# Optimization experiments

Hardware: AMD Instinct MI355X
Metric: run time of the kernel (lower is better)

Reference implementation:

```python
import jax, jax.numpy as jnp
import numpy as np
from jax import lax

B_SZ, C_IN, C_OUT, H_IM, W_IM = 2, 128, 128, 64, 64
N_STATE = 16
DT_RANK = 4  # ceil(128/32)


def _ln_cf(x, w, b, eps=1e-6):
    # channels_first LayerNorm over channel dim
    u = x.mean(1, keepdims=True)
    s = ((x - u) ** 2).mean(1, keepdims=True)
    return w[None, :, None, None] * (x - u) / jnp.sqrt(s + eps) + b[None, :, None, None]


def _bn_train(x, g, b, eps=1e-5):
    # BatchNorm2d in training mode (batch statistics, biased variance)
    m = x.mean((0, 2, 3), keepdims=True)
    v = ((x - m) ** 2).mean((0, 2, 3), keepdims=True)
    return g[None, :, None, None] * (x - m) / jnp.sqrt(v + eps) + b[None, :, None, None]


def _dwconv(x, w, b):
    y = lax.conv_general_dilated(x, w, (1, 1), 'SAME', feature_group_count=x.shape[1],
                                 dimension_numbers=('NCHW', 'OIHW', 'NCHW'))
    return y + b[None, :, None, None]


def _conv1x1(x, w, b):
    return jnp.einsum('oi,bihw->bohw', w, x) + b[None, :, None, None]


def _selective_scan(u, dt, A, Bm, Cm, D, delta_bias):
    # u, dt: [B,Ch,L]; A: [Ch,N]; Bm, Cm: [B,N,L]; D: [Ch]
    dt = jax.nn.softplus(dt + delta_bias[None, :, None])
    xs = (dt.transpose(2, 0, 1), u.transpose(2, 0, 1), Bm.transpose(2, 0, 1), Cm.transpose(2, 0, 1))
    h0 = jnp.zeros(u.shape[:2] + (A.shape[1],), u.dtype)

    def step(h, inp):
        dt_t, u_t, b_t, c_t = inp
        dA = jnp.exp(dt_t[..., None] * A)                        # [B,Ch,N]
        h = h * dA + (dt_t * u_t)[..., None] * b_t[:, None, :]   # [B,Ch,N]
        return h, jnp.einsum('bcn,bn->bc', h, c_t)

    _, ys = lax.scan(step, h0, xs)
    return ys.transpose(1, 2, 0) + u * D[None, :, None]


def _ssm_apply(u, Wx, bx, Wdt, bdt, Alog, D, r):
    # u: [B,Ch,L]. Replicates torch row-major .reshape of [(B L),D] -> [B,D,L].
    Bb, Ch, L = u.shape
    N = Alog.shape[1]
    x_flat = u.transpose(0, 2, 1).reshape(Bb * L, Ch)   # 'b c l -> (b l) c'
    x_dbl = x_flat @ Wx.T + bx
    dt = (x_dbl[:, :r] @ Wdt.T + bdt).reshape(Bb, Wdt.shape[0], L)
    Bm = x_dbl[:, r:r + N].reshape(Bb, N, L)
    Cm = x_dbl[:, r + N:].reshape(Bb, N, L)
    return _selective_scan(u, dt, -jnp.exp(Alog), Bm, Cm, D, bdt)


def _forward(x, ln_in_w, ln_in_b, inproj_w, inproj_b, ln_mamba_w, ln_mamba_b, convm_w, convm_b,
             convr_w, convr_b, ln_cat_w, ln_cat_b, xproj_f_w, xproj_f_b, dtproj_f_w, dtproj_f_b,
             Alog_f, D_f, xproj_b_w, xproj_b_b, dtproj_b_w, dtproj_b_b, Alog_b, D_b,
             xproj_u_w, xproj_u_b, dtproj_u_w, dtproj_u_b, Alog_u, D_u, gate1_w, gate1_b,
             bn_g, bn_b, gate2_w, gate2_b, outproj_w, outproj_b, outln_w, outln_b):
    Bb, C, H, W = x.shape
    L = H * W
    half = C // 2
    x = _ln_cf(x, ln_in_w, ln_in_b)
    xp = _conv1x1(x, inproj_w, inproj_b)
    x_mamba, x_res = xp[:, :C], xp[:, C:]
    x_mamba = _ln_cf(x_mamba, ln_mamba_w, ln_mamba_b)
    x_mamba = jax.nn.silu(_dwconv(x_mamba, convm_w, convm_b))
    x_res = jax.nn.silu(_dwconv(x_res, convr_w, convr_b))
    # forward scan on first half of channels
    xf = x_mamba[:, :half].reshape(Bb, half, L)
    yf = _ssm_apply(xf, xproj_f_w, xproj_f_b, dtproj_f_w, dtproj_f_b, Alog_f, D_f, DT_RANK).reshape(Bb, half, H, W)
    # backward scan on second half (flip H,W, scan, flip back)
    xb = x_mamba[:, half:][:, :, ::-1, ::-1]
    yb = _ssm_apply(xb.reshape(Bb, half, L), xproj_b_w, xproj_b_b, dtproj_b_w, dtproj_b_b,
                    Alog_b, D_b, DT_RANK).reshape(Bb, half, H, W)[:, :, ::-1, ::-1]
    concat = _ln_cf(jnp.concatenate([yf, yb], axis=1), ln_cat_w, ln_cat_b)
    # uncertainty-ordered scan on full x_mamba
    sig = jax.nn.sigmoid(x_mamba.mean(1, keepdims=True))
    unc = (-(sig * jnp.log(sig + 1e-6))).reshape(Bb, L)
    idx = jnp.argsort(-unc, axis=1)       # descending uncertainty
    inv = jnp.argsort(idx, axis=1)        # inverse permutation
    xs = jnp.take_along_axis(x_mamba.reshape(Bb, C, L), idx[:, None, :], axis=2)
    yu = _ssm_apply(xs, xproj_u_w, xproj_u_b, dtproj_u_w, dtproj_u_b, Alog_u, D_u, 2 * DT_RANK)
    yu = jnp.take_along_axis(yu, inv[:, None, :], axis=2).reshape(Bb, C, H, W)
    # gated fusion
    g = jax.nn.relu(_bn_train(_conv1x1(jnp.concatenate([concat, yu], 1), gate1_w, gate1_b), bn_g, bn_b))
    g = jax.nn.sigmoid(_conv1x1(g, gate2_w, gate2_b))
    fused = g * yu + (1.0 - g) * concat
    out = _conv1x1(jnp.concatenate([fused, x_res], 1), outproj_w, outproj_b)
    return _ln_cf(out, outln_w, outln_b)


def setup_inputs() -> dict:
    key = jax.random.key(0)
    ks = jax.random.split(key, 16)
    C, half, R, N = C_IN, C_IN // 2, DT_RANK, N_STATE
    rn = lambda k, shp, s=0.02: jax.random.normal(k, shp, jnp.float32) * s

    def inv_dt(k, n):
        dt = jnp.exp(jax.random.uniform(k, (n,)) * (np.log(0.1) - np.log(0.001)) + np.log(0.001))
        dt = jnp.maximum(dt, 1e-4)
        return dt + jnp.log(-jnp.expm1(-dt))

    std = R ** -0.5
    Alog_h = jnp.log(jnp.broadcast_to(jnp.arange(1, N + 1, dtype=jnp.float32), (half, N)))
    Alog_fl = jnp.log(jnp.broadcast_to(jnp.arange(1, N + 1, dtype=jnp.float32), (C, N)))
    return {
        'x': jax.random.normal(ks[0], (B_SZ, C, H_IM, W_IM), jnp.float32),
        'ln_in_w': jnp.ones(C), 'ln_in_b': jnp.zeros(C),
        'inproj_w': rn(ks[1], (2 * C, C)), 'inproj_b': jnp.zeros(2 * C),
        'ln_mamba_w': jnp.ones(C), 'ln_mamba_b': jnp.zeros(C),
        'convm_w': rn(ks[2], (C, 1, 3, 3), 0.1), 'convm_b': jnp.zeros(C),
        'convr_w': rn(ks[3], (C, 1, 3, 3), 0.1), 'convr_b': jnp.zeros(C),
        'ln_cat_w': jnp.ones(C), 'ln_cat_b': jnp.zeros(C),
        'xproj_f_w': rn(ks[4], (R + 2 * N, half)), 'xproj_f_b': jnp.zeros(R + 2 * N),
        'dtproj_f_w': jax.random.uniform(ks[5], (half, R), minval=-std, maxval=std),
        'dtproj_f_b': inv_dt(ks[6], half),
        'Alog_f': Alog_h, 'D_f': jnp.ones(half),
        'xproj_b_w': rn(ks[7], (R + 2 * N, half)), 'xproj_b_b': jnp.zeros(R + 2 * N),
        'dtproj_b_w': jax.random.uniform(ks[8], (half, R), minval=-std, maxval=std),
        'dtproj_b_b': inv_dt(ks[9], half),
        'Alog_b': Alog_h, 'D_b': jnp.ones(half),
        'xproj_u_w': rn(ks[10], (2 * R + 2 * N, C)), 'xproj_u_b': jnp.zeros(2 * R + 2 * N),
        'dtproj_u_w': jax.random.uniform(ks[11], (C, 2 * R), minval=-std, maxval=std),
        'dtproj_u_b': inv_dt(ks[12], C),
        'Alog_u': Alog_fl, 'D_u': jnp.ones(C),
        'gate1_w': rn(ks[13], (C, 2 * C)), 'gate1_b': jnp.zeros(C),
        'bn_g': jnp.ones(C), 'bn_b': jnp.zeros(C),
        'gate2_w': rn(ks[14], (C, C)), 'gate2_b': jnp.zeros(C),
        'outproj_w': rn(ks[15], (C_OUT, 2 * C)), 'outproj_b': jnp.zeros(C_OUT),
        'outln_w': jnp.ones(C_OUT), 'outln_b': jnp.zeros(C_OUT),
    }


def reference(x, ln_in_w, ln_in_b, inproj_w, inproj_b, ln_mamba_w, ln_mamba_b, convm_w, convm_b,
              convr_w, convr_b, ln_cat_w, ln_cat_b, xproj_f_w, xproj_f_b, dtproj_f_w, dtproj_f_b,
              Alog_f, D_f, xproj_b_w, xproj_b_b, dtproj_b_w, dtproj_b_b, Alog_b, D_b,
              xproj_u_w, xproj_u_b, dtproj_u_w, dtproj_u_b, Alog_u, D_u, gate1_w, gate1_b,
              bn_g, bn_b, gate2_w, gate2_b, outproj_w, outproj_b, outln_w, outln_b):
    return _forward(x, ln_in_w, ln_in_b, inproj_w, inproj_b, ln_mamba_w, ln_mamba_b, convm_w, convm_b,
                    convr_w, convr_b, ln_cat_w, ln_cat_b, xproj_f_w, xproj_f_b, dtproj_f_w, dtproj_f_b,
                    Alog_f, D_f, xproj_b_w, xproj_b_b, dtproj_b_w, dtproj_b_b, Alog_b, D_b,
                    xproj_u_w, xproj_u_b, dtproj_u_w, dtproj_u_b, Alog_u, D_u, gate1_w, gate1_b,
                    bn_g, bn_b, gate2_w, gate2_b, outproj_w, outproj_b, outln_w, outln_b)
```

## Files before the change

kernel.cpp:

```cpp
#include <hip/hip_runtime.h>
#include <cstdint>
#include <cstddef>

#define TPB 256

namespace {

constexpr int B_SZ = 2;
constexpr int C    = 128;
constexpr int HALF = 64;
constexpr int L    = 4096;
constexpr int N    = 16;
constexpr int HH   = 64;
constexpr int WW   = 64;

__device__ __forceinline__ float softplusf(float x) {
  return fmaxf(x, 0.f) + __logf(1.f + __expf(-fabsf(x)));
}
__device__ __forceinline__ float sigm(float x) { return 1.f / (1.f + __expf(-x)); }

__device__ __forceinline__ unsigned long long unc_key(float u, int i) {
  unsigned m = __float_as_uint(u);
  m = (m & 0x80000000u) ? ~m : (m | 0x80000000u);
  return ((unsigned long long)(~m) << 32) | (unsigned)i;
}

__global__ void k_conv_ln(const float* __restrict__ X, int bsX,
                          const float* __restrict__ lnw, const float* __restrict__ lnb,
                          const float* __restrict__ W, const float* __restrict__ bias,
                          float* __restrict__ Y, int I, int O,
                          float* __restrict__ st1s, float* __restrict__ st1q) {
  constexpr int O_PB = 8;
  __shared__ float Wl[O_PB * 128];
  __shared__ float aw[128], ab[128];
  const int o0 = blockIdx.y * O_PB;
  const int b  = blockIdx.z;
  for (int t = threadIdx.x; t < O_PB * I; t += TPB) {
    int i = t / O_PB, k = t % O_PB;
    Wl[t] = W[(size_t)(o0 + k) * I + i];
  }
  for (int t = threadIdx.x; t < I; t += TPB) { aw[t] = lnw[t]; ab[t] = lnb[t]; }
  __syncthreads();
  const int l0 = blockIdx.x * (2 * TPB) + threadIdx.x;
  const int l1 = l0 + TPB;
  const float* X0 = X + (size_t)b * bsX + l0;
  const float* X1 = X + (size_t)b * bsX + l1;
  float s0 = 0.f, q0 = 0.f, s1 = 0.f, q1 = 0.f;
#pragma unroll 8
  for (int i = 0; i < I; ++i) {
    float v0 = X0[(size_t)i * L], v1 = X1[(size_t)i * L];
    s0 += v0; q0 += v0 * v0; s1 += v1; q1 += v1 * v1;
  }
  const float m0 = s0 / I, m1 = s1 / I;
  const float r0 = rsqrtf(q0 / I - m0 * m0 + 1e-6f);
  const float r1 = rsqrtf(q1 / I - m1 * m1 + 1e-6f);
  float acc0[O_PB], acc1[O_PB];
#pragma unroll
  for (int k = 0; k < O_PB; ++k) { acc0[k] = bias[o0 + k]; acc1[k] = acc0[k]; }
#pragma unroll 4
  for (int i = 0; i < I; ++i) {
    float xv0 = (X0[(size_t)i * L] - m0) * r0 * aw[i] + ab[i];
    float xv1 = (X1[(size_t)i * L] - m1) * r1 * aw[i] + ab[i];
#pragma unroll
    for (int k = 0; k < O_PB; ++k) {
      acc0[k] += Wl[i * O_PB + k] * xv0;
      acc1[k] += Wl[i * O_PB + k] * xv1;
    }
  }
#pragma unroll
  for (int k = 0; k < O_PB; ++k) {
    Y[((size_t)b * O + o0 + k) * L + l0] = acc0[k];
    Y[((size_t)b * O + o0 + k) * L + l1] = acc1[k];
  }
  if (o0 < 128) {
    float ss0 = 0.f, qq0 = 0.f, ss1 = 0.f, qq1 = 0.f;
#pragma unroll
    for (int k = 0; k < O_PB; ++k) {
      ss0 += acc0[k]; qq0 += acc0[k] * acc0[k];
      ss1 += acc1[k]; qq1 += acc1[k] * acc1[k];
    }
    atomicAdd(&st1s[b * L + l0], ss0);
    atomicAdd(&st1q[b * L + l0], qq0);
    atomicAdd(&st1s[b * L + l1], ss1);
    atomicAdd(&st1q[b * L + l1], qq1);
  }
}

__global__ void k_dwconv_t(const float* __restrict__ xp,
                           const float* __restrict__ st1s, const float* __restrict__ st1q,
                           const float* __restrict__ lnw, const float* __restrict__ lnb,
                           const float* __restrict__ Wm, const float* __restrict__ bm,
                           const float* __restrict__ Wr, const float* __restrict__ br,
                           float* __restrict__ xm, float* __restrict__ xr) {
  const int c = blockIdx.y;
  const int z = blockIdx.z;
  const int b = z & 1, mode = z >> 1;
  const int h0 = blockIdx.x * 4;
  __shared__ float T[6][66];
  const float* Xc = xp + ((size_t)b * 2 * C + (mode ? C + c : c)) * L;
  const float lw = mode ? 0.f : lnw[c];
  const float lb2 = mode ? 0.f : lnb[c];
  for (int t = threadIdx.x; t < 6 * 66; t += TPB) {
    int r = t / 66, cc = t % 66 - 1;
    int hh = h0 - 1 + r;
    float v = 0.f;
    if (hh >= 0 && hh < HH && cc >= 0 && cc < WW) {
      int li = hh * WW + cc;
      v = Xc[li];
      if (mode == 0) {
        float sv = st1s[b * L + li], qv = st1q[b * L + li];
        float m = sv * (1.f / 128.f);
        float rr = rsqrtf(qv * (1.f / 128.f) - m * m + 1e-6f);
        v = (v - m) * rr * lw + lb2;
      }
    }
    T[r][t % 66] = v;
  }
  __syncthreads();
  const int hl = threadIdx.x >> 6, w = threadIdx.x & 63;
  const float* W9 = (mode ? Wr : Wm) + c * 9;
  float acc = mode ? br[c] : bm[c];
#pragma unroll
  for (int kh = 0; kh < 3; ++kh)
#pragma unroll
    for (int kw = 0; kw < 3; ++kw)
      acc += T[hl + kh][w + kw] * W9[kh * 3 + kw];
  const int l = (h0 + hl) * WW + w;
  float* Yp = mode ? xr : xm;
  Yp[((size_t)b * C + c) * L + l] = acc * sigm(acc);
}

__global__ void k_unc(const float* __restrict__ xm, float* __restrict__ unc) {
  const int lp = threadIdx.x & 63;
  const int wv = threadIdx.x >> 6;
  const int p  = blockIdx.x * 64 + lp;
  const int b = p / L, l = p % L;
  const float* Xp = xm + (size_t)b * C * L + l;
  float s = 0.f;
#pragma unroll 8
  for (int i = 0; i < 32; ++i) s += Xp[(size_t)(wv * 32 + i) * L];
  __shared__ float r1[4][64];
  r1[wv][lp] = s;
  __syncthreads();
  if (wv == 0) {
    float st = r1[0][lp] + r1[1][lp] + r1[2][lp] + r1[3][lp];
    float sg = sigm(st / C);
    unc[p] = -(sg * __logf(sg + 1e-6f));
  }
}

__global__ void k_rank(const float* __restrict__ unc, int* __restrict__ rankbuf) {
  constexpr int JC = 512;
  __shared__ unsigned long long K[JC];
  const int b  = blockIdx.z;
  const int j0 = blockIdx.y * JC;
  const int i  = blockIdx.x * TPB + threadIdx.x;
  for (int t = threadIdx.x; t < JC; t += TPB)
    K[t] = unc_key(unc[b * L + j0 + t], j0 + t);
  __syncthreads();
  const unsigned long long my = unc_key(unc[b * L + i], i);
  int cnt = 0;
#pragma unroll 8
  for (int j = 0; j < JC; ++j) cnt += (K[j] < my) ? 1 : 0;
  atomicAdd(&rankbuf[b * L + i], cnt);
}

__global__ void k_scatgath(const float* __restrict__ xm, const int* __restrict__ rankbuf,
                           float* __restrict__ xs, int* __restrict__ inv,
                           int* __restrict__ idx) {
  int t = blockIdx.x * TPB + threadIdx.x;
  int l = t % L, c = (t / L) % C, b = t / (C * L);
  int r = rankbuf[b * L + l];
  xs[((size_t)b * C + c) * L + r] = xm[t];
  if (c == 0) { inv[b * L + l] = r; idx[b * L + r] = l; }
}

__global__ void k_convx_all(const float* __restrict__ xm, const float* __restrict__ xs,
                            const float* __restrict__ Wf, const float* __restrict__ bf,
                            const float* __restrict__ Wb, const float* __restrict__ bb,
                            const float* __restrict__ Wu, const float* __restrict__ bu,
                            float* __restrict__ XDF, float* __restrict__ XDU) {
  const int z = blockIdx.z;
  const bool isU = z >= 4;
  const int I = isU ? 128 : 64;
  const int O = isU ? 40 : 36;
  const int o0 = blockIdx.y * 4;
  if (o0 >= O) return;
  int b, dir;
  const float *W, *bi;
  if (!isU) { dir = z >> 1; b = z & 1; W = dir ? Wb : Wf; bi = dir ? bb : bf; }
  else      { dir = 0; b = z - 4; W = Wu; bi = bu; }
  __shared__ float Wl[4 * 128];
  for (int t = threadIdx.x; t < 4 * I; t += TPB) {
    int i = t / 4, k = t % 4;
    Wl[t] = W[(size_t)(o0 + k) * I + i];
  }
  __syncthreads();
  const int l = blockIdx.x * TPB + threadIdx.x;
  const int ls = isU ? l : (dir ? (L - 1 - l) : l);
  const float* Xb = isU ? (xs + (size_t)b * C * L)
                        : (xm + ((size_t)b * C + dir * HALF) * L);
  float acc[4];
#pragma unroll
  for (int k = 0; k < 4; ++k) acc[k] = bi[o0 + k];
#pragma unroll 4
  for (int i = 0; i < I; ++i) {
    float xv = Xb[(size_t)i * L + ls];
#pragma unroll
    for (int k = 0; k < 4; ++k) acc[k] += Wl[i * 4 + k] * xv;
  }
  float* yp = isU ? (XDU + ((size_t)b * L + l) * 40 + o0)
                  : (XDF + ((size_t)z * L + l) * 36 + o0);
#pragma unroll
  for (int k = 0; k < 4; ++k) yp[k] = acc[k];
}

__global__ void k_bc_all(const float* __restrict__ xdblF, const float* __restrict__ xdblU,
                         float* __restrict__ BmTF, float* __restrict__ CmTF,
                         float* __restrict__ BmTU, float* __restrict__ CmTU) {
  const int z = blockIdx.z;
  const bool isU = z >= 4;
  const int RT = isU ? 8 : 4, OT = isU ? 40 : 36;
  const float* src = isU ? (xdblU + (size_t)(z - 4) * L * 40)
                         : (xdblF + (size_t)z * L * 36);
  float* BT = isU ? (BmTU + (size_t)(z - 4) * L * N) : (BmTF + (size_t)z * L * N);
  float* CT = isU ? (CmTU + (size_t)(z - 4) * L * N) : (CmTF + (size_t)z * L * N);
  const int n = blockIdx.y;
  const int l2 = blockIdx.x * TPB + threadIdx.x;
  int f2 = n * L + l2;
  int lb = f2 >> 4, cb = f2 & 15;
  const float* xr2 = src + (size_t)lb * OT + RT + cb;
  size_t ob = (size_t)l2 * N + n;
  BT[ob] = xr2[0];
  CT[ob] = xr2[N];
}

__global__ __launch_bounds__(1024) void
k_scan_all(const float* __restrict__ xdblF, const float* __restrict__ xdblU,
           const float* __restrict__ dtf_w, const float* __restrict__ dtf_b,
           const float* __restrict__ dtb_w, const float* __restrict__ dtb_b,
           const float* __restrict__ dtu_w, const float* __restrict__ dtu_b,
           const float* __restrict__ xm, const float* __restrict__ xs,
           const int* __restrict__ idx,
           const float* __restrict__ BmTF, const float* __restrict__ CmTF,
           const float* __restrict__ BmTU, const float* __restrict__ CmTU,
           const float* __restrict__ Alog_f, const float* __restrict__ Alog_b,
           const float* __restrict__ Alog_u,
           const float* __restrict__ D_f, const float* __restrict__ D_b,
           const float* __restrict__ D_u,
           float* __restrict__ yf, float* __restrict__ yb, float* __restrict__ yu) {
  const int blk = blockIdx.x;
  const int tid = threadIdx.x;
  const bool isU = blk >= 256;
  int CsT, RT, c, b, dir;
  const float *Wdt, *bdt, *Alog, *Dv, *xdbl, *BT, *CT, *Ub;
  const int* idxb = nullptr;
  float* Y;
  int OT;
  if (!isU) {
    CsT = 64; RT = 4; OT = 36;
    int zb = blk >> 6; c = blk & 63; dir = zb >> 1; b = zb & 1;
    Wdt = dir ? dtb_w : dtf_w; bdt = dir ? dtb_b : dtf_b;
    Alog = dir ? Alog_b : Alog_f; Dv = dir ? D_b : D_f;
    xdbl = xdblF + (size_t)zb * L * 36;
    BT = BmTF + (size_t)zb * L * N; CT = CmTF + (size_t)zb * L * N;
    Ub = xm + ((size_t)b * C + dir * HALF + c) * L;
    Y = (dir ? yb : yf) + ((size_t)b * HALF + c) * L;
  } else {
    CsT = 128; RT = 8; OT = 40;
    int blk2 = blk - 256; b = blk2 >> 7; c = blk2 & 127; dir = 0;
    Wdt = dtu_w; bdt = dtu_b; Alog = Alog_u; Dv = D_u;
    xdbl = xdblU + (size_t)b * L * 40;
    BT = BmTU + (size_t)b * L * N; CT = CmTU + (size_t)b * L * N;
    Ub = xs + ((size_t)b * C + c) * L;
    idxb = idx + b * L;
    Y = yu + ((size_t)b * C + c) * L;
  }
  __shared__ float sW[1024];
  __shared__ float sb2[128];
  __shared__ float4 dtL4[64 * 17];
  __shared__ float4 uL4[64 * 17];
  __shared__ float sA[N][65], sH[N][65];
  for (int t = tid; t < CsT * RT; t += 1024) {
    int csrc = t / RT, r = t % RT;
    sW[r * CsT + csrc] = Wdt[t];
  }
  for (int t = tid; t < CsT; t += 1024) sb2[t] = bdt[t];
  __syncthreads();
  {
    const int chunk_d = tid >> 4;
    const int sq4 = tid & 15;
    const int sq = sq4 * 4;
    const int lsrc = isU ? (c * 32 + (chunk_d >> 1)) : (c * 64 + chunk_d);
    const float* xrp = xdbl + (size_t)lsrc * OT;
    float xr[8];
    for (int r = 0; r < RT; ++r) xr[r] = xrp[r];
    const float bcc = sb2[c];
    float dv[4], uv[4];
#pragma unroll
    for (int j = 0; j < 4; ++j) {
      int s = sq + j;
      int csrc = isU ? (((chunk_d & 1) << 6) + s) : s;
      float acc = sb2[csrc] + bcc;
      for (int r = 0; r < RT; ++r) acc += sW[r * CsT + csrc] * xr[r];
      int l = (chunk_d << 6) + s;
      dv[j] = softplusf(acc);
      uv[j] = Ub[isU ? l : (dir ? (L - 1 - l) : l)];
    }
    dtL4[chunk_d * 17 + sq4] = make_float4(dv[0], dv[1], dv[2], dv[3]);
    uL4[chunk_d * 17 + sq4]  = make_float4(uv[0], uv[1], uv[2], uv[3]);
  }
  __syncthreads();
  const int n = tid & 15;
  const int chunk = tid >> 4;
  const float a = -__expf(Alog[c * N + n]);
  const float* bp = BT + ((size_t)(chunk << 6)) * N + n;
  const float* cp = CT + ((size_t)(chunk << 6)) * N + n;
  float ap = 1.f, h = 0.f;
#pragma unroll 4
  for (int m = 0; m < 16; ++m) {
    float4 d4 = dtL4[chunk * 17 + m];
    float4 u4 = uL4[chunk * 17 + m];
    float dv[4] = {d4.x, d4.y, d4.z, d4.w};
    float uv[4] = {u4.x, u4.y, u4.z, u4.w};
#pragma unroll
    for (int jj = 0; jj < 4; ++jj) {
      int s = (m << 2) + jj;
      float bn = bp[(size_t)s * N];
      float dA = __expf(dv[jj] * a);
      ap *= dA;
      h = h * dA + dv[jj] * uv[jj] * bn;
    }
  }
  sA[n][chunk] = ap; sH[n][chunk] = h;
  __syncthreads();
  {
    const int w = tid >> 6;
    const int k = tid & 63;
    float A = sA[w][k];
    float Bv = sH[w][k];
#pragma unroll
    for (int j = 1; j < 64; j <<= 1) {
      float pa = __shfl_up(A, j);
      float pb = __shfl_up(Bv, j);
      if (k >= j) { Bv = pb * A + Bv; A = pa * A; }
    }
    float hprev = __shfl_up(Bv, 1);
    sH[w][k] = (k == 0) ? 0.f : hprev;
  }
  __syncthreads();
  h = sH[n][chunk];
  const float Dc = Dv[c];
  const float* uLrow = (const float*)&uL4[chunk * 17];
  const bool h1 = (n & 1) != 0, h2 = (n & 2) != 0, h3 = (n & 4) != 0, h4 = (n & 8) != 0;
  float ybuf[4];
#pragma unroll
  for (int q = 0; q < 4; ++q) {
    float v[16];
#pragma unroll
    for (int m = 0; m < 4; ++m) {
      float4 d4 = dtL4[chunk * 17 + (q << 2) + m];
      float4 u4 = uL4[chunk * 17 + (q << 2) + m];
      float dv[4] = {d4.x, d4.y, d4.z, d4.w};
      float uv[4] = {u4.x, u4.y, u4.z, u4.w};
#pragma unroll
      for (int jj = 0; jj < 4; ++jj) {
        int s = (q << 4) + (m << 2) + jj;
        float bn = bp[(size_t)s * N];
        float cn = cp[(size_t)s * N];
        float dA = __expf(dv[jj] * a);
        h = h * dA + dv[jj] * uv[jj] * bn;
        v[(m << 2) + jj] = h * cn;
      }
    }
    float u8[8];
#pragma unroll
    for (int k2 = 0; k2 < 8; ++k2) {
      float snd = h1 ? v[2 * k2] : v[2 * k2 + 1];
      float t = __shfl_xor(snd, 1);
      u8[k2] = (h1 ? v[2 * k2 + 1] : v[2 * k2]) + t;
    }
    float u4a[4];
#pragma unroll
    for (int k2 = 0; k2 < 4; ++k2) {
      float snd = h2 ? u8[2 * k2] : u8[2 * k2 + 1];
      float t = __shfl_xor(snd, 2);
      u4a[k2] = (h2 ? u8[2 * k2 + 1] : u8[2 * k2]) + t;
    }
    float u2a[2];
#pragma unroll
    for (int k2 = 0; k2 < 2; ++k2) {
      float snd = h3 ? u4a[2 * k2] : u4a[2 * k2 + 1];
      float t = __shfl_xor(snd, 4);
      u2a[k2] = (h3 ? u4a[2 * k2 + 1] : u4a[2 * k2]) + t;
    }
    float snd = h4 ? u2a[0] : u2a[1];
    float t = __shfl_xor(snd, 8);
    float ysum = (h4 ? u2a[1] : u2a[0]) + t;
    float myu = uLrow[(q << 4) + n];
    ybuf[q] = ysum + myu * Dc;
  }
  if (!isU) {
    float* Yp = Y + (chunk << 6);
#pragma unroll
    for (int q = 0; q < 4; ++q) Yp[16 * q + n] = ybuf[q];
  } else {
    const int s0 = chunk << 6;
#pragma unroll
    for (int q = 0; q < 4; ++q) Y[idxb[s0 + 16 * q + n]] = ybuf[q];
  }
}

template <int O_PB>
__global__ void k_gate1(const float* __restrict__ yf, const float* __restrict__ yb,
                        const float* __restrict__ lncw, const float* __restrict__ lncb,
                        const float* __restrict__ yu,
                        const float* __restrict__ W, const float* __restrict__ bias,
                        float* __restrict__ g1,
                        float* __restrict__ st2m, float* __restrict__ st2r,
                        float* __restrict__ bnsum) {
  __shared__ float Wl[O_PB * 256];
  __shared__ float cw[128], cb2[128];
  __shared__ float part[2][O_PB][4];
  const int o0 = blockIdx.y * O_PB;
  const int b  = blockIdx.z;
  for (int t = threadIdx.x; t < O_PB * 256; t += TPB) {
    int i = t / O_PB, k = t % O_PB;
    Wl[t] = W[(size_t)(o0 + k) * 256 + i];
  }
  for (int t = threadIdx.x; t < 128; t += TPB) { cw[t] = lncw[t]; cb2[t] = lncb[t]; }
  __syncthreads();
  const int l = blockIdx.x * TPB + threadIdx.x;
  const float* f0 = yf + (size_t)b * HALF * L + l;
  const float* b0 = yb + (size_t)b * HALF * L + (L - 1 - l);
  const float* u0 = yu + (size_t)b * C * L + l;
  float s = 0.f, s2 = 0.f;
#pragma unroll 8
  for (int i = 0; i < 64; ++i) { float v = f0[(size_t)i * L]; s += v; s2 += v * v; }
#pragma unroll 8
  for (int i = 0; i < 64; ++i) { float v = b0[(size_t)i * L]; s += v; s2 += v * v; }
  const float m = s / C;
  const float r = rsqrtf(s2 / C - m * m + 1e-6f);
  if (blockIdx.y == 0) { st2m[b * L + l] = m; st2r[b * L + l] = r; }
  float acc[O_PB];
#pragma unroll
  for (int k = 0; k < O_PB; ++k) acc[k] = bias[o0 + k];
#pragma unroll 4
  for (int i = 0; i < 64; ++i) {
    float cv = (f0[(size_t)i * L] - m) * r * cw[i] + cb2[i];
#pragma unroll
    for (int k = 0; k < O_PB; ++k) acc[k] += Wl[i * O_PB + k] * cv;
  }
#pragma unroll 4
  for (int i = 0; i < 64; ++i) {
    float cv = (b0[(size_t)i * L] - m) * r * cw[64 + i] + cb2[64 + i];
#pragma unroll
    for (int k = 0; k < O_PB; ++k) acc[k] += Wl[(64 + i) * O_PB + k] * cv;
  }
#pragma unroll 4
  for (int i = 0; i < 128; ++i) {
    float xv = u0[(size_t)i * L];
#pragma unroll
    for (int k = 0; k < O_PB; ++k) acc[k] += Wl[(128 + i) * O_PB + k] * xv;
  }
#pragma unroll
  for (int k = 0; k < O_PB; ++k)
    g1[((size_t)b * C + o0 + k) * L + l] = acc[k];
  const int wv = threadIdx.x >> 6, lnn = threadIdx.x & 63;
#pragma unroll
  for (int k = 0; k < O_PB; ++k) {
    float v = acc[k];
    v += __shfl_xor(v, 1);  v += __shfl_xor(v, 2);  v += __shfl_xor(v, 4);
    v += __shfl_xor(v, 8);  v += __shfl_xor(v, 16); v += __shfl_xor(v, 32);
    if (lnn == 0) part[0][k][wv] = v;
    float q = acc[k] * acc[k];
    q += __shfl_xor(q, 1);  q += __shfl_xor(q, 2);  q += __shfl_xor(q, 4);
    q += __shfl_xor(q, 8);  q += __shfl_xor(q, 16); q += __shfl_xor(q, 32);
    if (lnn == 0) part[1][k][wv] = q;
  }
  __syncthreads();
  if (threadIdx.x < 2 * O_PB) {
    int which = threadIdx.x >= O_PB, k = threadIdx.x % O_PB;
    float v = part[which][k][0] + part[which][k][1] + part[which][k][2] + part[which][k][3];
    atomicAdd(&bnsum[which * 128 + o0 + k], v);
  }
}

template <int O_PB>
__global__ void k_gate2_fuse(const float* __restrict__ g1,
                             const float* __restrict__ bnsum,
                             const float* __restrict__ bn_g, const float* __restrict__ bn_b,
                             const float* __restrict__ W, const float* __restrict__ bias,
                             const float* __restrict__ yu,
                             const float* __restrict__ yf, const float* __restrict__ yb,
                             const float* __restrict__ mean2, const float* __restrict__ rinv2,
                             const float* __restrict__ lncw, const float* __restrict__ lncb,
                             float* __restrict__ fused) {
  __shared__ float Wl[O_PB * 128];
  __shared__ float sc[128], sh[128];
  __shared__ float cwo[O_PB], cbo[O_PB];
  const int o0 = blockIdx.y * O_PB;
  const int b  = blockIdx.z;
  for (int t = threadIdx.x; t < O_PB * 128; t += TPB) {
    int i = t / O_PB, k = t % O_PB;
    Wl[t] = W[(size_t)(o0 + k) * 128 + i];
  }
  for (int t = threadIdx.x; t < 128; t += TPB) {
    float sv = bnsum[t], qv = bnsum[128 + t];
    float mean = sv / (B_SZ * L);
    float var  = qv / (B_SZ * L) - mean * mean;
    float scv = bn_g[t] * rsqrtf(var + 1e-5f);
    sc[t] = scv;
    sh[t] = bn_b[t] - mean * scv;
  }
  if (threadIdx.x < O_PB) {
    cwo[threadIdx.x] = lncw[o0 + threadIdx.x];
    cbo[threadIdx.x] = lncb[o0 + threadIdx.x];
  }
  __syncthreads();
  const int l = blockIdx.x * TPB + threadIdx.x;
  const float m = mean2[b * L + l], r = rinv2[b * L + l];
  const float* Xb = g1 + (size_t)b * C * L + l;
  float acc[O_PB];
#pragma unroll
  for (int k = 0; k < O_PB; ++k) acc[k] = bias[o0 + k];
#pragma unroll 4
  for (int i = 0; i < 128; ++i) {
    float v = fmaxf(Xb[(size_t)i * L] * sc[i] + sh[i], 0.f);
#pragma unroll
    for (int k = 0; k < O_PB; ++k) acc[k] += Wl[i * O_PB + k] * v;
  }
#pragma unroll
  for (int k = 0; k < O_PB; ++k) {
    int o = o0 + k;
    float g = sigm(acc[k]);
    float yuv = yu[((size_t)b * C + o) * L + l];
    float yv = (o < 64) ? yf[((size_t)b * HALF + o) * L + l]
                        : yb[((size_t)b * HALF + (o - 64)) * L + (L - 1 - l)];
    float cv = (yv - m) * r * cwo[k] + cbo[k];
    fused[((size_t)b * C + o) * L + l] = g * yuv + (1.f - g) * cv;
  }
}

template <int O_PB>
__global__ void k_conv1x1_cat2(const float* __restrict__ X1, const float* __restrict__ X2,
                               const float* __restrict__ W, const float* __restrict__ bias,
                               float* __restrict__ Y, int O) {
  __shared__ float Wl[O_PB * 256];
  const int o0 = blockIdx.y * O_PB;
  const int b  = blockIdx.z;
  for (int t = threadIdx.x; t < O_PB * 256; t += TPB) {
    int i = t / O_PB, k = t % O_PB;
    Wl[t] = W[(size_t)(o0 + k) * 256 + i];
  }
  __syncthreads();
  const int l = blockIdx.x * TPB + threadIdx.x;
  const float* Xb1 = X1 + (size_t)b * C * L + l;
  const float* Xb2 = X2 + (size_t)b * C * L + l;
  float acc[O_PB];
#pragma unroll
  for (int k = 0; k < O_PB; ++k) acc[k] = bias[o0 + k];
#pragma unroll 4
  for (int i = 0; i < 128; ++i) {
    float xv = Xb1[(size_t)i * L];
#pragma unroll
    for (int k = 0; k < O_PB; ++k) acc[k] += Wl[i * O_PB + k] * xv;
  }
#pragma unroll 4
  for (int i = 0; i < 128; ++i) {
    float xv = Xb2[(size_t)i * L];
#pragma unroll
    for (int k = 0; k < O_PB; ++k) acc[k] += Wl[(128 + i) * O_PB + k] * xv;
  }
#pragma unroll
  for (int k = 0; k < O_PB; ++k)
    Y[((size_t)b * O + o0 + k) * L + l] = acc[k];
}

__global__ void k_ln_cf(const float* __restrict__ X,
                        const float* __restrict__ w, const float* __restrict__ bchan,
                        float* __restrict__ Y) {
  const int lp = threadIdx.x & 63;
  const int wv = threadIdx.x >> 6;
  const int p  = blockIdx.x * 64 + lp;
  const int b = p / L, l = p % L;
  const float* Xp = X + (size_t)b * C * L + l;
  float s = 0.f, s2 = 0.f;
#pragma unroll 8
  for (int i = 0; i < 32; ++i) {
    float v = Xp[(size_t)(wv * 32 + i) * L];
    s += v; s2 += v * v;
  }
  __shared__ float r1[4][64], r2[4][64];
  r1[wv][lp] = s; r2[wv][lp] = s2;
  __syncthreads();
  float st  = r1[0][lp] + r1[1][lp] + r1[2][lp] + r1[3][lp];
  float s2t = r2[0][lp] + r2[1][lp] + r2[2][lp] + r2[3][lp];
  float mean = st / C;
  float rinv = rsqrtf(s2t / C - mean * mean + 1e-6f);
  float* Yp = Y + (size_t)b * C * L + l;
#pragma unroll 8
  for (int i = 0; i < 32; ++i) {
    int c = wv * 32 + i;
    float v = Xp[(size_t)c * L];
    Yp[(size_t)c * L] = w[c] * (v - mean) * rinv + bchan[c];
  }
}

}

extern "C" void kernel_launch(void* const* d_in, const int* in_sizes, int n_in,
                              void* d_out, int out_size, void* d_ws, size_t ws_size,
                              hipStream_t stream) {
  const float* x         = (const float*)d_in[0];
  const float* ln_in_w   = (const float*)d_in[1];
  const float* ln_in_b   = (const float*)d_in[2];
  const float* inproj_w  = (const float*)d_in[3];
  const float* inproj_b  = (const float*)d_in[4];
  const float* ln_m_w    = (const float*)d_in[5];
  const float* ln_m_b    = (const float*)d_in[6];
  const float* convm_w   = (const float*)d_in[7];
  const float* convm_b   = (const float*)d_in[8];
  const float* convr_w   = (const float*)d_in[9];
  const float* convr_b   = (const float*)d_in[10];
  const float* ln_cat_w  = (const float*)d_in[11];
  const float* ln_cat_b  = (const float*)d_in[12];
  const float* xpf_w     = (const float*)d_in[13];
  const float* xpf_b     = (const float*)d_in[14];
  const float* dtf_w     = (const float*)d_in[15];
  const float* dtf_b     = (const float*)d_in[16];
  const float* Alog_f    = (const float*)d_in[17];
  const float* D_f       = (const float*)d_in[18];
  const float* xpb_w     = (const float*)d_in[19];
  const float* xpb_b     = (const float*)d_in[20];
  const float* dtb_w     = (const float*)d_in[21];
  const float* dtb_b     = (const float*)d_in[22];
  const float* Alog_b    = (const float*)d_in[23];
  const float* D_b       = (const float*)d_in[24];
  const float* xpu_w     = (const float*)d_in[25];
  const float* xpu_b     = (const float*)d_in[26];
  const float* dtu_w     = (const float*)d_in[27];
  const float* dtu_b     = (const float*)d_in[28];
  const float* Alog_u    = (const float*)d_in[29];
  const float* D_u       = (const float*)d_in[30];
  const float* gate1_w   = (const float*)d_in[31];
  const float* gate1_b   = (const float*)d_in[32];
  const float* bn_g      = (const float*)d_in[33];
  const float* bn_b      = (const float*)d_in[34];
  const float* gate2_w   = (const float*)d_in[35];
  const float* gate2_b   = (const float*)d_in[36];
  const float* outproj_w = (const float*)d_in[37];
  const float* outproj_b = (const float*)d_in[38];
  const float* outln_w   = (const float*)d_in[39];
  const float* outln_b   = (const float*)d_in[40];

  float* ws = (float*)d_ws;
  size_t off = 0;
  auto alloc = [&](size_t n) { float* p = ws + off; off += n; return p; };

  const size_t BL = (size_t)B_SZ * L;
  float* st1s  = alloc(BL);
  float* st1q  = alloc(BL);
  int*   rank  = (int*)alloc(BL);
  float* bnsum = alloc(256);
  const size_t zeroBytes = (3 * BL + 256) * sizeof(float);

  float* xp    = alloc((size_t)B_SZ * 2 * C * L);
  float* xm    = alloc((size_t)B_SZ * C * L);
  float* xr    = alloc((size_t)B_SZ * C * L);
  float* unc   = alloc(BL);
  int*   inv   = (int*)alloc(BL);
  int*   idx   = (int*)alloc(BL);
  float* xs    = alloc((size_t)B_SZ * C * L);
  float* xdblF = alloc((size_t)4 * L * 36);
  float* BmTF  = alloc((size_t)4 * L * N);
  float* CmTF  = alloc((size_t)4 * L * N);
  float* xdblU = alloc((size_t)2 * L * 40);
  float* BmTU  = alloc((size_t)2 * L * N);
  float* CmTU  = alloc((size_t)2 * L * N);
  float* yf    = alloc((size_t)B_SZ * HALF * L);
  float* yb    = alloc((size_t)B_SZ * HALF * L);
  float* yu    = alloc((size_t)B_SZ * C * L);
  float* st2m  = alloc(BL);
  float* st2r  = alloc(BL);
  float* g1    = alloc((size_t)B_SZ * C * L);
  float* fused = alloc((size_t)B_SZ * C * L);
  float* outp  = alloc((size_t)B_SZ * C * L);
  (void)ws_size; (void)in_sizes; (void)n_in; (void)out_size;

  const int pixB = B_SZ * L / 64;
  const int elemB = B_SZ * C * L / TPB;

  hipMemsetAsync(st1s, 0, zeroBytes, stream);
  k_conv_ln<<<dim3(L / (2 * TPB), 32, B_SZ), TPB, 0, stream>>>(
      x, C * L, ln_in_w, ln_in_b, inproj_w, inproj_b, xp, 128, 256, st1s, st1q);
  k_dwconv_t<<<dim3(HH / 4, C, 2 * B_SZ), TPB, 0, stream>>>(
      xp, st1s, st1q, ln_m_w, ln_m_b, convm_w, convm_b, convr_w, convr_b, xm, xr);
  k_unc<<<pixB, TPB, 0, stream>>>(xm, unc);
  k_rank<<<dim3(L / TPB, 8, B_SZ), TPB, 0, stream>>>(unc, rank);
  k_scatgath<<<elemB, TPB, 0, stream>>>(xm, rank, xs, inv, idx);
  k_convx_all<<<dim3(L / TPB, 10, 6), TPB, 0, stream>>>(
      xm, xs, xpf_w, xpf_b, xpb_w, xpb_b, xpu_w, xpu_b, xdblF, xdblU);
  k_bc_all<<<dim3(L / TPB, N, 6), TPB, 0, stream>>>(
      xdblF, xdblU, BmTF, CmTF, BmTU, CmTU);
  k_scan_all<<<512, 1024, 0, stream>>>(
      xdblF, xdblU, dtf_w, dtf_b, dtb_w, dtb_b, dtu_w, dtu_b,
      xm, xs, idx, BmTF, CmTF, BmTU, CmTU,
      Alog_f, Alog_b, Alog_u, D_f, D_b, D_u, yf, yb, yu);
  k_gate1<8><<<dim3(L / TPB, 16, B_SZ), TPB, 0, stream>>>(
      yf, yb, ln_cat_w, ln_cat_b, yu, gate1_w, gate1_b, g1, st2m, st2r, bnsum);
  k_gate2_fuse<8><<<dim3(L / TPB, 16, B_SZ), TPB, 0, stream>>>(
      g1, bnsum, bn_g, bn_b, gate2_w, gate2_b, yu, yf, yb, st2m, st2r,
      ln_cat_w, ln_cat_b, fused);
  k_conv1x1_cat2<8><<<dim3(L / TPB, 16, B_SZ), TPB, 0, stream>>>(
      fused, xr, outproj_w, outproj_b, outp, 128);
  k_ln_cf<<<pixB, TPB, 0, stream>>>(outp, outln_w, outln_b, (float*)d_out);
}
```

Baseline: 331.9 us.

## Fuse output LayerNorm stats into outproj, widen convx outputs, split unc reduction

Result: no change. 330.1 us (-0.5%).

```diff
diff --git a/kernel.cpp b/kernel.cpp
--- a/kernel.cpp
+++ b/kernel.cpp
@@ -131,19 +131,21 @@
 }
 
 __global__ void k_unc(const float* __restrict__ xm, float* __restrict__ unc) {
-  const int lp = threadIdx.x & 63;
-  const int wv = threadIdx.x >> 6;
-  const int p  = blockIdx.x * 64 + lp;
+  const int lp = threadIdx.x & 31;
+  const int g  = threadIdx.x >> 5;
+  const int p  = blockIdx.x * 32 + lp;
   const int b = p / L, l = p % L;
   const float* Xp = xm + (size_t)b * C * L + l;
   float s = 0.f;
 #pragma unroll 8
-  for (int i = 0; i < 32; ++i) s += Xp[(size_t)(wv * 32 + i) * L];
-  __shared__ float r1[4][64];
-  r1[wv][lp] = s;
-  __syncthreads();
-  if (wv == 0) {
-    float st = r1[0][lp] + r1[1][lp] + r1[2][lp] + r1[3][lp];
+  for (int i = 0; i < 16; ++i) s += Xp[(size_t)(g * 16 + i) * L];
+  __shared__ float r1[8][32];
+  r1[g][lp] = s;
+  __syncthreads();
+  if (g == 0) {
+    float st = 0.f;
+#pragma unroll
+    for (int j = 0; j < 8; ++j) st += r1[j][lp];
     float sg = sigm(st / C);
     unc[p] = -(sg * __logf(sg + 1e-6f));
   }
@@ -180,39 +182,41 @@
                             const float* __restrict__ Wb, const float* __restrict__ bb,
                             const float* __restrict__ Wu, const float* __restrict__ bu,
                             float* __restrict__ XDF, float* __restrict__ XDU) {
+  constexpr int O_PB = 8;
   const int z = blockIdx.z;
   const bool isU = z >= 4;
   const int I = isU ? 128 : 64;
   const int O = isU ? 40 : 36;
-  const int o0 = blockIdx.y * 4;
+  const int o0 = blockIdx.y * O_PB;
   if (o0 >= O) return;
   int b, dir;
   const float *W, *bi;
   if (!isU) { dir = z >> 1; b = z & 1; W = dir ? Wb : Wf; bi = dir ? bb : bf; }
   else      { dir = 0; b = z - 4; W = Wu; bi = bu; }
-  __shared__ float Wl[4 * 128];
-  for (int t = threadIdx.x; t < 4 * I; t += TPB) {
-    int i = t / 4, k = t % 4;
-    Wl[t] = W[(size_t)(o0 + k) * I + i];
+  __shared__ float Wl[O_PB * 128];
+  for (int t = threadIdx.x; t < O_PB * I; t += TPB) {
+    int i = t / O_PB, k = t % O_PB;
+    Wl[t] = (o0 + k < O) ? W[(size_t)(o0 + k) * I + i] : 0.f;
   }
   __syncthreads();
   const int l = blockIdx.x * TPB + threadIdx.x;
   const int ls = isU ? l : (dir ? (L - 1 - l) : l);
   const float* Xb = isU ? (xs + (size_t)b * C * L)
                         : (xm + ((size_t)b * C + dir * HALF) * L);
-  float acc[4];
-#pragma unroll
-  for (int k = 0; k < 4; ++k) acc[k] = bi[o0 + k];
+  float acc[O_PB];
+#pragma unroll
+  for (int k = 0; k < O_PB; ++k) acc[k] = (o0 + k < O) ? bi[o0 + k] : 0.f;
 #pragma unroll 4
   for (int i = 0; i < I; ++i) {
     float xv = Xb[(size_t)i * L + ls];
 #pragma unroll
-    for (int k = 0; k < 4; ++k) acc[k] += Wl[i * 4 + k] * xv;
+    for (int k = 0; k < O_PB; ++k) acc[k] += Wl[i * O_PB + k] * xv;
   }
   float* yp = isU ? (XDU + ((size_t)b * L + l) * 40 + o0)
                   : (XDF + ((size_t)z * L + l) * 36 + o0);
 #pragma unroll
-  for (int k = 0; k < 4; ++k) yp[k] = acc[k];
+  for (int k = 0; k < O_PB; ++k)
+    if (o0 + k < O) yp[k] = acc[k];
 }
 
 __global__ void k_bc_all(const float* __restrict__ xdblF, const float* __restrict__ xdblU,
@@ -545,7 +549,8 @@
 template <int O_PB>
 __global__ void k_conv1x1_cat2(const float* __restrict__ X1, const float* __restrict__ X2,
                                const float* __restrict__ W, const float* __restrict__ bias,
-                               float* __restrict__ Y, int O) {
+                               float* __restrict__ Y, int O,
+                               float* __restrict__ st3s, float* __restrict__ st3q) {
   __shared__ float Wl[O_PB * 256];
   const int o0 = blockIdx.y * O_PB;
   const int b  = blockIdx.z;
@@ -575,36 +580,22 @@
 #pragma unroll
   for (int k = 0; k < O_PB; ++k)
     Y[((size_t)b * O + o0 + k) * L + l] = acc[k];
-}
-
-__global__ void k_ln_cf(const float* __restrict__ X,
-                        const float* __restrict__ w, const float* __restrict__ bchan,
-                        float* __restrict__ Y) {
-  const int lp = threadIdx.x & 63;
-  const int wv = threadIdx.x >> 6;
-  const int p  = blockIdx.x * 64 + lp;
-  const int b = p / L, l = p % L;
-  const float* Xp = X + (size_t)b * C * L + l;
-  float s = 0.f, s2 = 0.f;
-#pragma unroll 8
-  for (int i = 0; i < 32; ++i) {
-    float v = Xp[(size_t)(wv * 32 + i) * L];
-    s += v; s2 += v * v;
-  }
-  __shared__ float r1[4][64], r2[4][64];
-  r1[wv][lp] = s; r2[wv][lp] = s2;
-  __syncthreads();
-  float st  = r1[0][lp] + r1[1][lp] + r1[2][lp] + r1[3][lp];
-  float s2t = r2[0][lp] + r2[1][lp] + r2[2][lp] + r2[3][lp];
-  float mean = st / C;
-  float rinv = rsqrtf(s2t / C - mean * mean + 1e-6f);
-  float* Yp = Y + (size_t)b * C * L + l;
-#pragma unroll 8
-  for (int i = 0; i < 32; ++i) {
-    int c = wv * 32 + i;
-    float v = Xp[(size_t)c * L];
-    Yp[(size_t)c * L] = w[c] * (v - mean) * rinv + bchan[c];
-  }
+  float ss = 0.f, qq = 0.f;
+#pragma unroll
+  for (int k = 0; k < O_PB; ++k) { ss += acc[k]; qq += acc[k] * acc[k]; }
+  atomicAdd(&st3s[b * L + l], ss);
+  atomicAdd(&st3q[b * L + l], qq);
+}
+
+__global__ void k_ln_fin(const float* __restrict__ X,
+                         const float* __restrict__ st3s, const float* __restrict__ st3q,
+                         const float* __restrict__ w, const float* __restrict__ bchan,
+                         float* __restrict__ Y) {
+  int t = blockIdx.x * TPB + threadIdx.x;
+  int l = t % L, c = (t / L) % C, b = t / (C * L);
+  float m = st3s[b * L + l] * (1.f / 128.f);
+  float rinv = rsqrtf(st3q[b * L + l] * (1.f / 128.f) - m * m + 1e-6f);
+  Y[t] = w[c] * (X[t] - m) * rinv + bchan[c];
 }
 
 }
@@ -662,8 +653,10 @@
   float* st1s  = alloc(BL);
   float* st1q  = alloc(BL);
   int*   rank  = (int*)alloc(BL);
+  float* st3s  = alloc(BL);
+  float* st3q  = alloc(BL);
   float* bnsum = alloc(256);
-  const size_t zeroBytes = (3 * BL + 256) * sizeof(float);
+  const size_t zeroBytes = (5 * BL + 256) * sizeof(float);
 
   float* xp    = alloc((size_t)B_SZ * 2 * C * L);
   float* xm    = alloc((size_t)B_SZ * C * L);
@@ -688,7 +681,6 @@
   float* outp  = alloc((size_t)B_SZ * C * L);
   (void)ws_size; (void)in_sizes; (void)n_in; (void)out_size;
 
-  const int pixB = B_SZ * L / 64;
   const int elemB = B_SZ * C * L / TPB;
 
   hipMemsetAsync(st1s, 0, zeroBytes, stream);
@@ -696,10 +688,10 @@
       x, C * L, ln_in_w, ln_in_b, inproj_w, inproj_b, xp, 128, 256, st1s, st1q);
   k_dwconv_t<<<dim3(HH / 4, C, 2 * B_SZ), TPB, 0, stream>>>(
       xp, st1s, st1q, ln_m_w, ln_m_b, convm_w, convm_b, convr_w, convr_b, xm, xr);
-  k_unc<<<pixB, TPB, 0, stream>>>(xm, unc);
+  k_unc<<<B_SZ * L / 32, TPB, 0, stream>>>(xm, unc);
   k_rank<<<dim3(L / TPB, 8, B_SZ), TPB, 0, stream>>>(unc, rank);
   k_scatgath<<<elemB, TPB, 0, stream>>>(xm, rank, xs, inv, idx);
-  k_convx_all<<<dim3(L / TPB, 10, 6), TPB, 0, stream>>>(
+  k_convx_all<<<dim3(L / TPB, 5, 6), TPB, 0, stream>>>(
       xm, xs, xpf_w, xpf_b, xpb_w, xpb_b, xpu_w, xpu_b, xdblF, xdblU);
   k_bc_all<<<dim3(L / TPB, N, 6), TPB, 0, stream>>>(
       xdblF, xdblU, BmTF, CmTF, BmTU, CmTU);
@@ -713,6 +705,7 @@
       g1, bnsum, bn_g, bn_b, gate2_w, gate2_b, yu, yf, yb, st2m, st2r,
       ln_cat_w, ln_cat_b, fused);
   k_conv1x1_cat2<8><<<dim3(L / TPB, 16, B_SZ), TPB, 0, stream>>>(
-      fused, xr, outproj_w, outproj_b, outp, 128);
-  k_ln_cf<<<pixB, TPB, 0, stream>>>(outp, outln_w, outln_b, (float*)d_out);
-}
+      fused, xr, outproj_w, outproj_b, outp, 128, st3s, st3q);
+  k_ln_fin<<<elemB, TPB, 0, stream>>>(outp, st3s, st3q, outln_w, outln_b,
+                                      (float*)d_out);
+}
```
